# Kernel optimization log

Measured on AMD Instinct MI355X. Metric: run time of the kernel, lower is better.

Reference implementation:

```python
import jax, jax.numpy as jnp
import numpy as np

N_NODES = 10000
N_EDGES = 640000
HIDDEN = 128
N_LAYERS = 3
DECAY_RATE = 1.0


def setup_inputs() -> dict:
    key = jax.random.key(0)
    ks = jax.random.split(key, 16)
    D, L = HIDDEN, N_LAYERS
    s = 1.0 / np.sqrt(D)
    inp = {
        "x": jax.random.normal(ks[0], (N_NODES, D), dtype=jnp.float32),
        "edge_index": jax.random.randint(ks[1], (2, N_EDGES), 0, N_NODES, dtype=jnp.int32),
        "confidences": jax.random.uniform(ks[2], (N_NODES,), dtype=jnp.float32),
        # per-layer message MLP params, stacked over layers: [L, D, D] / [L, D]
        "msg_W1": jax.random.normal(ks[3], (L, D, D), dtype=jnp.float32) * s,
        "msg_b1": jnp.zeros((L, D), dtype=jnp.float32),
        "msg_W2": jax.random.normal(ks[4], (L, D, D), dtype=jnp.float32) * s,
        "msg_b2": jnp.zeros((L, D), dtype=jnp.float32),
        # per-layer self MLP params
        "self_W1": jax.random.normal(ks[5], (L, D, D), dtype=jnp.float32) * s,
        "self_b1": jnp.zeros((L, D), dtype=jnp.float32),
        "self_W2": jax.random.normal(ks[6], (L, D, D), dtype=jnp.float32) * s,
        "self_b2": jnp.zeros((L, D), dtype=jnp.float32),
        # layer-importance score net: Linear(D,D) -> ReLU -> Linear(D,1)
        "score_W1": jax.random.normal(ks[7], (D, D), dtype=jnp.float32) * s,
        "score_b1": jnp.zeros((D,), dtype=jnp.float32),
        "score_W2": jax.random.normal(ks[8], (D, 1), dtype=jnp.float32) * s,
        "score_b2": jnp.zeros((1,), dtype=jnp.float32),
    }
    return inp


def _mlp2(h, W1, b1, W2, b2):
    return jax.nn.relu(h @ W1 + b1) @ W2 + b2


def reference(x, edge_index, confidences,
              msg_W1, msg_b1, msg_W2, msg_b2,
              self_W1, self_b1, self_W2, self_b2,
              score_W1, score_b1, score_W2, score_b2):
    src, dst = edge_index[0], edge_index[1]
    # confidence-weighted edge weights: exp(-decay * |c_src - c_dst|)
    edge_weights = jnp.exp(-DECAY_RATE * jnp.abs(confidences[src] - confidences[dst]))  # [E]

    h = x
    layer_outputs = []
    for i in range(N_LAYERS):
        messages = _mlp2(h[src], msg_W1[i], msg_b1[i], msg_W2[i], msg_b2[i])  # [E, D]
        messages = messages * edge_weights[:, None]
        aggr = jax.ops.segment_sum(messages, dst, num_segments=N_NODES)  # [N, D]
        self_loop = _mlp2(h, self_W1[i], self_b1[i], self_W2[i], self_b2[i])
        h = jax.nn.relu(aggr + self_loop)  # dropout is identity in eval mode
        layer_outputs.append(h)

    stacked = jnp.stack(layer_outputs, axis=0)  # [L, N, D]
    scores = _mlp2(stacked, score_W1, score_b1, score_W2, score_b2)[..., 0]  # [L, N]
    layer_weights = jax.nn.softmax(scores, axis=0)  # softmax over layers
    output = jnp.sum(layer_weights[:, :, None] * stacked, axis=0)  # [N, D]
    return output, stacked, layer_weights
```

## Files before the change

kernel.cpp:

```cpp
#include <hip/hip_runtime.h>

#define NN 10000
#define NE 640000
#define D 128
#define NF (NN * D)
#define WS 136
#define CAP 128
#define GMB 157
#define GE ((NE + 255) / 256)
#define NAGG (NN / 4)
#define NDZ ((NN + 255) / 256)

typedef __bf16 bf16x8 __attribute__((ext_vector_type(8)));
typedef float f32x4 __attribute__((ext_vector_type(4)));


__global__ __launch_bounds__(256) void prep_kernel(
    const float* __restrict__ mW1, const float* __restrict__ mW2,
    const float* __restrict__ sW1, const float* __restrict__ sW2,
    const float* __restrict__ scW1, __bf16* __restrict__ wt, int* __restrict__ deg) {
    int b = blockIdx.x, t = threadIdx.x;
    if (b < 13) {
        int m = b;
        const float* W = (m < 3)   ? mW1 + (size_t)m * D * D
                       : (m < 6)   ? mW2 + (size_t)(m - 3) * D * D
                       : (m < 9)   ? sW1 + (size_t)(m - 6) * D * D
                       : (m < 12)  ? sW2 + (size_t)(m - 9) * D * D
                                   : scW1;
        __bf16* o = wt + (size_t)m * D * WS;
        for (int i = t; i < D * D; i += 256) {
            int k = i >> 7, n = i & 127;
            o[n * WS + k] = (__bf16)W[i];
        }
    } else {
        int i = (b - 13) * 256 + t;
        if (i < NN) deg[i] = 0;
    }
}


__device__ __forceinline__ void mlp_nostage_body(
    const __bf16* __restrict__ Abf, const float* __restrict__ Af32,
    const __bf16* __restrict__ Wt1, const float* __restrict__ b1,
    const __bf16* __restrict__ Wt2, const float* __restrict__ b2,
    __bf16* __restrict__ Mbf, float* __restrict__ Cself, int write_bf,
    __bf16 (*Tl)[16 * WS], int bx, int t) {
    int wid = t >> 6, lane = t & 63;
    int m16 = lane & 15, q = lane >> 4;
    int row0 = bx * 64 + wid * 16;
    int arow = min(row0 + m16, NN - 1);

    bf16x8 af[4];
    if (Af32) {
#pragma unroll
        for (int kk = 0; kk < 4; kk++) {
            const float4* pa = (const float4*)&Af32[(size_t)arow * D + kk * 32 + q * 8];
            float4 v0 = pa[0], v1 = pa[1];
            bf16x8 f;
            f[0] = (__bf16)v0.x; f[1] = (__bf16)v0.y; f[2] = (__bf16)v0.z; f[3] = (__bf16)v0.w;
            f[4] = (__bf16)v1.x; f[5] = (__bf16)v1.y; f[6] = (__bf16)v1.z; f[7] = (__bf16)v1.w;
            af[kk] = f;
        }
    } else {
#pragma unroll
        for (int kk = 0; kk < 4; kk++)
            af[kk] = *(const bf16x8*)&Abf[(size_t)arow * D + kk * 32 + q * 8];
    }
    float b1v[8], b2v[8];
#pragma unroll
    for (int ct = 0; ct < 8; ct++) { b1v[ct] = b1[ct * 16 + m16]; b2v[ct] = b2[ct * 16 + m16]; }

    f32x4 acc[8];
#pragma unroll
    for (int ct = 0; ct < 8; ct++) acc[ct] = (f32x4){0.f, 0.f, 0.f, 0.f};
#pragma unroll
    for (int kk = 0; kk < 4; kk++) {
#pragma unroll
        for (int ct = 0; ct < 8; ct++) {
            bf16x8 bb = *(const bf16x8*)&Wt1[(ct * 16 + m16) * WS + kk * 32 + q * 8];
            acc[ct] = __builtin_amdgcn_mfma_f32_16x16x32_bf16(af[kk], bb, acc[ct], 0, 0, 0);
        }
    }
#pragma unroll
    for (int ct = 0; ct < 8; ct++) {
#pragma unroll
        for (int r = 0; r < 4; r++) {
            float v = fmaxf(acc[ct][r] + b1v[ct], 0.f);
            Tl[wid][(q * 4 + r) * WS + ct * 16 + m16] = (__bf16)v;
        }
    }
#pragma unroll
    for (int ct = 0; ct < 8; ct++) acc[ct] = (f32x4){0.f, 0.f, 0.f, 0.f};
#pragma unroll
    for (int kk = 0; kk < 4; kk++) {
        bf16x8 a = *(const bf16x8*)&Tl[wid][m16 * WS + kk * 32 + q * 8];
#pragma unroll
        for (int ct = 0; ct < 8; ct++) {
            bf16x8 bb = *(const bf16x8*)&Wt2[(ct * 16 + m16) * WS + kk * 32 + q * 8];
            acc[ct] = __builtin_amdgcn_mfma_f32_16x16x32_bf16(a, bb, acc[ct], 0, 0, 0);
        }
    }
    if (write_bf) {
#pragma unroll
        for (int ct = 0; ct < 8; ct++) {
#pragma unroll
            for (int r = 0; r < 4; r++) {
                int row = row0 + q * 4 + r;
                if (row < NN) Mbf[(size_t)row * D + ct * 16 + m16] = (__bf16)(acc[ct][r] + b2v[ct]);
            }
        }
    } else {
#pragma unroll
        for (int ct = 0; ct < 8; ct++) {
#pragma unroll
            for (int r = 0; r < 4; r++) {
                int row = row0 + q * 4 + r;
                if (row < NN) Cself[(size_t)row * D + ct * 16 + m16] = acc[ct][r] + b2v[ct];
            }
        }
    }
}


__global__ __launch_bounds__(256) void scatter_mlp0_kernel(
    const int* __restrict__ ei, const float* __restrict__ conf,
    int* __restrict__ deg, float2* __restrict__ meta,
    const float* __restrict__ x,
    const __bf16* __restrict__ Wt1m, const float* __restrict__ b1m,
    const __bf16* __restrict__ Wt2m, const float* __restrict__ b2m, __bf16* __restrict__ Mbf,
    const __bf16* __restrict__ Wt1s, const float* __restrict__ b1s,
    const __bf16* __restrict__ Wt2s, const float* __restrict__ b2s, float* __restrict__ Cself) {
    __shared__ __align__(16) __bf16 Tl[4][16 * WS];
    int b = blockIdx.x, t = threadIdx.x;
    if (b < GMB) {
        mlp_nostage_body(nullptr, x, Wt1m, b1m, Wt2m, b2m, Mbf, nullptr, 1, Tl, b, t);
        return;
    }
    if (b < 2 * GMB) {
        mlp_nostage_body(nullptr, x, Wt1s, b1s, Wt2s, b2s, nullptr, Cself, 0, Tl, b - GMB, t);
        return;
    }
    int e = (b - 2 * GMB) * 256 + t;
    if (e < NE) {
        int s = ei[e];
        int d = ei[NE + e];
        float w = expf(-fabsf(conf[s] - conf[d]));
        int r = atomicAdd(&deg[d], 1);
        if (r < CAP) meta[(size_t)d * CAP + r] = make_float2(__int_as_float(s), w);
    }
}


__global__ __launch_bounds__(256) void aggregate_kernel(
    const uint4* __restrict__ Mbf4, const float4* __restrict__ Mself4,
    const int* __restrict__ deg, const float2* __restrict__ meta,
    float4* __restrict__ out4, bf16x8* __restrict__ stbf8) {
    int wid = (blockIdx.x * 256 + threadIdx.x) >> 6;
    int lane = threadIdx.x & 63;
    int q = lane >> 4, l4 = lane & 15, l5 = lane & 31;
    int dg = min(deg[wid], CAP);
    size_t beg = (size_t)wid * CAP;
    float a[8] = {0.f, 0.f, 0.f, 0.f, 0.f, 0.f, 0.f, 0.f};
    float2 mcur = meta[beg + l5];
    for (int rel = 0; rel < dg; rel += 32) {
        float2 mnext = meta[beg + rel + 32 + l5];
        int srcid[8];
        float wgt[8];
#pragma unroll
        for (int u = 0; u < 8; u++) {
            int sl = 4 * u + q;
            int sid = __float_as_int(__shfl(mcur.x, sl));
            float w = __shfl(mcur.y, sl);
            bool valid = (rel + sl) < dg;
            srcid[u] = valid ? sid : 0;
            wgt[u] = valid ? w : 0.f;
        }
        uint4 g[8];
#pragma unroll
        for (int u = 0; u < 8; u++) g[u] = Mbf4[(size_t)srcid[u] * 16 + l4];
#pragma unroll
        for (int u = 0; u < 8; u++) {
            float w = wgt[u];
            a[0] = fmaf(w, __uint_as_float(g[u].x << 16), a[0]);
            a[1] = fmaf(w, __uint_as_float(g[u].x & 0xFFFF0000u), a[1]);
            a[2] = fmaf(w, __uint_as_float(g[u].y << 16), a[2]);
            a[3] = fmaf(w, __uint_as_float(g[u].y & 0xFFFF0000u), a[3]);
            a[4] = fmaf(w, __uint_as_float(g[u].z << 16), a[4]);
            a[5] = fmaf(w, __uint_as_float(g[u].z & 0xFFFF0000u), a[5]);
            a[6] = fmaf(w, __uint_as_float(g[u].w << 16), a[6]);
            a[7] = fmaf(w, __uint_as_float(g[u].w & 0xFFFF0000u), a[7]);
        }
        mcur = mnext;
    }
#pragma unroll
    for (int i = 0; i < 8; i++) {
        a[i] += __shfl_xor(a[i], 16);
        a[i] += __shfl_xor(a[i], 32);
    }
    if (q == 0) {
        float4 sv0 = Mself4[(size_t)wid * 32 + 2 * l4];
        float4 sv1 = Mself4[(size_t)wid * 32 + 2 * l4 + 1];
        float4 r0, r1;
        r0.x = fmaxf(a[0] + sv0.x, 0.f);
        r0.y = fmaxf(a[1] + sv0.y, 0.f);
        r0.z = fmaxf(a[2] + sv0.z, 0.f);
        r0.w = fmaxf(a[3] + sv0.w, 0.f);
        r1.x = fmaxf(a[4] + sv1.x, 0.f);
        r1.y = fmaxf(a[5] + sv1.y, 0.f);
        r1.z = fmaxf(a[6] + sv1.z, 0.f);
        r1.w = fmaxf(a[7] + sv1.w, 0.f);
        out4[(size_t)wid * 32 + 2 * l4] = r0;
        out4[(size_t)wid * 32 + 2 * l4 + 1] = r1;
        bf16x8 hb;
        hb[0] = (__bf16)r0.x; hb[1] = (__bf16)r0.y;
        hb[2] = (__bf16)r0.z; hb[3] = (__bf16)r0.w;
        hb[4] = (__bf16)r1.x; hb[5] = (__bf16)r1.y;
        hb[6] = (__bf16)r1.z; hb[7] = (__bf16)r1.w;
        stbf8[(size_t)wid * 16 + l4] = hb;
    }
}


__global__ __launch_bounds__(256) void mlp_pair_mfma(
    const __bf16* __restrict__ Abf,
    const __bf16* __restrict__ Wt1a, const float* __restrict__ b1a,
    const __bf16* __restrict__ Wt2a, const float* __restrict__ b2a, __bf16* __restrict__ Mbf,
    const __bf16* __restrict__ Wt1b, const float* __restrict__ b1b,
    const __bf16* __restrict__ Wt2b, const float* __restrict__ b2b, float* __restrict__ Cself) {
    __shared__ __align__(16) __bf16 Tl[4][16 * WS];
    int pb = blockIdx.y;
    mlp_nostage_body(Abf, nullptr,
                     pb ? Wt1b : Wt1a, pb ? b1b : b1a,
                     pb ? Wt2b : Wt2a, pb ? b2b : b2a,
                     Mbf, Cself, pb == 0, Tl, blockIdx.x, threadIdx.x);
}


__global__ __launch_bounds__(256) void score_finalize_mfma(
    const __bf16* __restrict__ stbf, const float* __restrict__ st,
    const __bf16* __restrict__ Wt1, const float* __restrict__ b1,
    const float* __restrict__ w2, const float* __restrict__ b2,
    float* __restrict__ out, float* __restrict__ lw_out) {
    __shared__ float sc_l[3][64];
    __shared__ float lw_l[3][64];
    int t = threadIdx.x;
    int wid = t >> 6, lane = t & 63;
    int m16 = lane & 15, q = lane >> 4;
    int row0 = blockIdx.x * 64;

    int arow = min(row0 + wid * 16 + m16, NN - 1);
    float bb = b2[0];

    for (int l = 0; l < 3; l++) {
        const __bf16* A = stbf + (size_t)l * NF;
        f32x4 acc[8];
#pragma unroll
        for (int ct = 0; ct < 8; ct++) acc[ct] = (f32x4){0.f, 0.f, 0.f, 0.f};
#pragma unroll
        for (int kk = 0; kk < 4; kk++) {
            bf16x8 a = *(const bf16x8*)&A[(size_t)arow * D + kk * 32 + q * 8];
#pragma unroll
            for (int ct = 0; ct < 8; ct++) {
                bf16x8 b = *(const bf16x8*)&Wt1[(ct * 16 + m16) * WS + kk * 32 + q * 8];
                acc[ct] = __builtin_amdgcn_mfma_f32_16x16x32_bf16(a, b, acc[ct], 0, 0, 0);
            }
        }
        float p[4] = {0.f, 0.f, 0.f, 0.f};
#pragma unroll
        for (int ct = 0; ct < 8; ct++) {
            float bv = b1[ct * 16 + m16];
            float wv = w2[ct * 16 + m16];
#pragma unroll
            for (int r = 0; r < 4; r++) p[r] += fmaxf(acc[ct][r] + bv, 0.f) * wv;
        }
#pragma unroll
        for (int r = 0; r < 4; r++) {
#pragma unroll
            for (int off = 1; off < 16; off <<= 1) p[r] += __shfl_xor(p[r], off);
            if (m16 == 0) sc_l[l][wid * 16 + q * 4 + r] = p[r] + bb;
        }
    }
    __syncthreads();

    if (t < 64) {
        int row = row0 + t;
        float s0 = sc_l[0][t], s1 = sc_l[1][t], s2 = sc_l[2][t];
        float m = fmaxf(s0, fmaxf(s1, s2));
        float e0 = expf(s0 - m), e1 = expf(s1 - m), e2 = expf(s2 - m);
        float inv = 1.f / (e0 + e1 + e2);
        lw_l[0][t] = e0 * inv;
        lw_l[1][t] = e1 * inv;
        lw_l[2][t] = e2 * inv;
        if (row < NN) {
            lw_out[row] = e0 * inv;
            lw_out[NN + row] = e1 * inv;
            lw_out[2 * NN + row] = e2 * inv;
        }
    }
    __syncthreads();

    for (int i = t; i < 64 * 32; i += 256) {
        int r = i >> 5, c4 = i & 31;
        int row = row0 + r;
        if (row >= NN) break;
        float4 v0 = ((const float4*)(st + (size_t)row * D))[c4];
        float4 v1 = ((const float4*)(st + (size_t)NF + (size_t)row * D))[c4];
        float4 v2 = ((const float4*)(st + 2 * (size_t)NF + (size_t)row * D))[c4];
        float w0 = lw_l[0][r], w1 = lw_l[1][r], w2v = lw_l[2][r];
        float4 o;
        o.x = w0 * v0.x + w1 * v1.x + w2v * v2.x;
        o.y = w0 * v0.y + w1 * v1.y + w2v * v2.y;
        o.z = w0 * v0.z + w1 * v1.z + w2v * v2.z;
        o.w = w0 * v0.w + w1 * v1.w + w2v * v2.w;
        ((float4*)(out + (size_t)row * D))[c4] = o;
    }
}

extern "C" void kernel_launch(void* const* d_in, const int* in_sizes, int n_in,
                              void* d_out, int out_size, void* d_ws, size_t ws_size,
                              hipStream_t stream) {
    const float* x = (const float*)d_in[0];
    const int* ei = (const int*)d_in[1];
    const float* conf = (const float*)d_in[2];
    const float* msg_W1 = (const float*)d_in[3];
    const float* msg_b1 = (const float*)d_in[4];
    const float* msg_W2 = (const float*)d_in[5];
    const float* msg_b2 = (const float*)d_in[6];
    const float* self_W1 = (const float*)d_in[7];
    const float* self_b1 = (const float*)d_in[8];
    const float* self_W2 = (const float*)d_in[9];
    const float* self_b2 = (const float*)d_in[10];
    const float* score_W1 = (const float*)d_in[11];
    const float* score_b1 = (const float*)d_in[12];
    const float* score_W2 = (const float*)d_in[13];
    const float* score_b2 = (const float*)d_in[14];

    float* out = (float*)d_out;
    float* out_stacked = out + NF;
    float* out_lw = out + 4 * (size_t)NF;

    float* w = (float*)d_ws;
    float* Mself = w;
    float2* meta = (float2*)(w + (size_t)NF);
    __bf16* stbf = (__bf16*)(meta + (size_t)NN * CAP + 64);
    __bf16* Mbf = stbf + 3 * (size_t)NF;
    __bf16* wt = Mbf + (size_t)NF;
    int* deg = (int*)(wt + 13 * (size_t)D * WS);

    const size_t MAT = (size_t)D * WS;

    prep_kernel<<<13 + NDZ, 256, 0, stream>>>(
        msg_W1, msg_W2, self_W1, self_W2, score_W1, wt, deg);
    scatter_mlp0_kernel<<<2 * GMB + GE, 256, 0, stream>>>(
        ei, conf, deg, meta, x,
        wt + 0 * MAT, msg_b1, wt + 3 * MAT, msg_b2, Mbf,
        wt + 6 * MAT, self_b1, wt + 9 * MAT, self_b2, Mself);
    aggregate_kernel<<<NAGG, 256, 0, stream>>>(
        (const uint4*)Mbf, (const float4*)Mself, deg, meta,
        (float4*)(out_stacked + 0 * (size_t)NF), (bf16x8*)(stbf + 0 * (size_t)NF));
    for (int l = 1; l < 3; l++) {
        const __bf16* a_in = stbf + (size_t)(l - 1) * NF;
        mlp_pair_mfma<<<dim3(GMB, 2), 256, 0, stream>>>(
            a_in,
            wt + (size_t)l * MAT, msg_b1 + (size_t)l * D,
            wt + (size_t)(3 + l) * MAT, msg_b2 + (size_t)l * D, Mbf,
            wt + (size_t)(6 + l) * MAT, self_b1 + (size_t)l * D,
            wt + (size_t)(9 + l) * MAT, self_b2 + (size_t)l * D, Mself);
        aggregate_kernel<<<NAGG, 256, 0, stream>>>(
            (const uint4*)Mbf, (const float4*)Mself, deg, meta,
            (float4*)(out_stacked + (size_t)l * NF),
            (bf16x8*)(stbf + (size_t)l * NF));
    }
    score_finalize_mfma<<<GMB, 256, 0, stream>>>(
        stbf, out_stacked, wt + 12 * MAT, score_b1, score_W2, score_b2, out, out_lw);
}
```

Baseline: 238.6 us.

## Split aggregation in halves and overlap second half with next-layer MLP

Each layer's aggregation is split into two node halves. The second half runs in the same launch as the next layer's MLP (or the score pass) for the nodes already finished by the first half, and the remaining MLP or score blocks run in a follow-up kernel. Message and self-loop buffers are double-buffered so the next layer's outputs do not overwrite inputs the concurrent aggregation still reads. This is meant to fill idle CUs and hide the tail of the latency-bound gather kernel, at the cost of more launches and extra workspace.

Result: slower. 257.6 us (+8.0%).

```diff
diff --git a/kernel.cpp b/kernel.cpp
--- a/kernel.cpp
+++ b/kernel.cpp
@@ -7,8 +7,9 @@
 #define WS 136
 #define CAP 128
 #define GMB 157
+#define GMA 78
 #define GE ((NE + 255) / 256)
-#define NAGG (NN / 4)
+#define NAGH 1250
 #define NDZ ((NN + 255) / 256)
 
 typedef __bf16 bf16x8 __attribute__((ext_vector_type(8)));
@@ -122,41 +123,12 @@
 }
 
 
-__global__ __launch_bounds__(256) void scatter_mlp0_kernel(
-    const int* __restrict__ ei, const float* __restrict__ conf,
-    int* __restrict__ deg, float2* __restrict__ meta,
-    const float* __restrict__ x,
-    const __bf16* __restrict__ Wt1m, const float* __restrict__ b1m,
-    const __bf16* __restrict__ Wt2m, const float* __restrict__ b2m, __bf16* __restrict__ Mbf,
-    const __bf16* __restrict__ Wt1s, const float* __restrict__ b1s,
-    const __bf16* __restrict__ Wt2s, const float* __restrict__ b2s, float* __restrict__ Cself) {
-    __shared__ __align__(16) __bf16 Tl[4][16 * WS];
-    int b = blockIdx.x, t = threadIdx.x;
-    if (b < GMB) {
-        mlp_nostage_body(nullptr, x, Wt1m, b1m, Wt2m, b2m, Mbf, nullptr, 1, Tl, b, t);
-        return;
-    }
-    if (b < 2 * GMB) {
-        mlp_nostage_body(nullptr, x, Wt1s, b1s, Wt2s, b2s, nullptr, Cself, 0, Tl, b - GMB, t);
-        return;
-    }
-    int e = (b - 2 * GMB) * 256 + t;
-    if (e < NE) {
-        int s = ei[e];
-        int d = ei[NE + e];
-        float w = expf(-fabsf(conf[s] - conf[d]));
-        int r = atomicAdd(&deg[d], 1);
-        if (r < CAP) meta[(size_t)d * CAP + r] = make_float2(__int_as_float(s), w);
-    }
-}
-
-
-__global__ __launch_bounds__(256) void aggregate_kernel(
+__device__ __forceinline__ void aggregate_body(
     const uint4* __restrict__ Mbf4, const float4* __restrict__ Mself4,
     const int* __restrict__ deg, const float2* __restrict__ meta,
-    float4* __restrict__ out4, bf16x8* __restrict__ stbf8) {
-    int wid = (blockIdx.x * 256 + threadIdx.x) >> 6;
-    int lane = threadIdx.x & 63;
+    float4* __restrict__ out4, bf16x8* __restrict__ stbf8, int node0, int b, int t) {
+    int wid = node0 + ((b * 256 + t) >> 6);
+    int lane = t & 63;
     int q = lane >> 4, l4 = lane & 15, l5 = lane & 31;
     int dg = min(deg[wid], CAP);
     size_t beg = (size_t)wid * CAP;
@@ -221,33 +193,15 @@
 }
 
 
-__global__ __launch_bounds__(256) void mlp_pair_mfma(
-    const __bf16* __restrict__ Abf,
-    const __bf16* __restrict__ Wt1a, const float* __restrict__ b1a,
-    const __bf16* __restrict__ Wt2a, const float* __restrict__ b2a, __bf16* __restrict__ Mbf,
-    const __bf16* __restrict__ Wt1b, const float* __restrict__ b1b,
-    const __bf16* __restrict__ Wt2b, const float* __restrict__ b2b, float* __restrict__ Cself) {
-    __shared__ __align__(16) __bf16 Tl[4][16 * WS];
-    int pb = blockIdx.y;
-    mlp_nostage_body(Abf, nullptr,
-                     pb ? Wt1b : Wt1a, pb ? b1b : b1a,
-                     pb ? Wt2b : Wt2a, pb ? b2b : b2a,
-                     Mbf, Cself, pb == 0, Tl, blockIdx.x, threadIdx.x);
-}
-
-
-__global__ __launch_bounds__(256) void score_finalize_mfma(
+__device__ __forceinline__ void score_body(
+    int vb, int t, float* sc_l, float* lw_l,
     const __bf16* __restrict__ stbf, const float* __restrict__ st,
     const __bf16* __restrict__ Wt1, const float* __restrict__ b1,
     const float* __restrict__ w2, const float* __restrict__ b2,
     float* __restrict__ out, float* __restrict__ lw_out) {
-    __shared__ float sc_l[3][64];
-    __shared__ float lw_l[3][64];
-    int t = threadIdx.x;
     int wid = t >> 6, lane = t & 63;
     int m16 = lane & 15, q = lane >> 4;
-    int row0 = blockIdx.x * 64;
-
+    int row0 = vb * 64;
     int arow = min(row0 + wid * 16 + m16, NN - 1);
     float bb = b2[0];
 
@@ -277,20 +231,20 @@
         for (int r = 0; r < 4; r++) {
 #pragma unroll
             for (int off = 1; off < 16; off <<= 1) p[r] += __shfl_xor(p[r], off);
-            if (m16 == 0) sc_l[l][wid * 16 + q * 4 + r] = p[r] + bb;
+            if (m16 == 0) sc_l[l * 64 + wid * 16 + q * 4 + r] = p[r] + bb;
         }
     }
     __syncthreads();
 
     if (t < 64) {
         int row = row0 + t;
-        float s0 = sc_l[0][t], s1 = sc_l[1][t], s2 = sc_l[2][t];
+        float s0 = sc_l[0 * 64 + t], s1 = sc_l[1 * 64 + t], s2 = sc_l[2 * 64 + t];
         float m = fmaxf(s0, fmaxf(s1, s2));
         float e0 = expf(s0 - m), e1 = expf(s1 - m), e2 = expf(s2 - m);
         float inv = 1.f / (e0 + e1 + e2);
-        lw_l[0][t] = e0 * inv;
-        lw_l[1][t] = e1 * inv;
-        lw_l[2][t] = e2 * inv;
+        lw_l[0 * 64 + t] = e0 * inv;
+        lw_l[1 * 64 + t] = e1 * inv;
+        lw_l[2 * 64 + t] = e2 * inv;
         if (row < NN) {
             lw_out[row] = e0 * inv;
             lw_out[NN + row] = e1 * inv;
@@ -306,7 +260,7 @@
         float4 v0 = ((const float4*)(st + (size_t)row * D))[c4];
         float4 v1 = ((const float4*)(st + (size_t)NF + (size_t)row * D))[c4];
         float4 v2 = ((const float4*)(st + 2 * (size_t)NF + (size_t)row * D))[c4];
-        float w0 = lw_l[0][r], w1 = lw_l[1][r], w2v = lw_l[2][r];
+        float w0 = lw_l[0 * 64 + r], w1 = lw_l[1 * 64 + r], w2v = lw_l[2 * 64 + r];
         float4 o;
         o.x = w0 * v0.x + w1 * v1.x + w2v * v2.x;
         o.y = w0 * v0.y + w1 * v1.y + w2v * v2.y;
@@ -314,6 +268,115 @@
         o.w = w0 * v0.w + w1 * v1.w + w2v * v2.w;
         ((float4*)(out + (size_t)row * D))[c4] = o;
     }
+}
+
+
+__global__ __launch_bounds__(256) void scatter_mlp0_kernel(
+    const int* __restrict__ ei, const float* __restrict__ conf,
+    int* __restrict__ deg, float2* __restrict__ meta,
+    const float* __restrict__ x,
+    const __bf16* __restrict__ wt, const float* __restrict__ b1m, const float* __restrict__ b2m,
+    const float* __restrict__ b1s, const float* __restrict__ b2s,
+    __bf16* __restrict__ Mbf, float* __restrict__ Cself) {
+    __shared__ __align__(16) __bf16 Tl[4][16 * WS];
+    const size_t MAT = (size_t)D * WS;
+    int b = blockIdx.x, t = threadIdx.x;
+    if (b < GMB) {
+        mlp_nostage_body(nullptr, x, wt + 0 * MAT, b1m, wt + 3 * MAT, b2m,
+                         Mbf, nullptr, 1, Tl, b, t);
+        return;
+    }
+    if (b < 2 * GMB) {
+        mlp_nostage_body(nullptr, x, wt + 6 * MAT, b1s, wt + 9 * MAT, b2s,
+                         nullptr, Cself, 0, Tl, b - GMB, t);
+        return;
+    }
+    int e = (b - 2 * GMB) * 256 + t;
+    if (e < NE) {
+        int s = ei[e];
+        int d = ei[NE + e];
+        float w = expf(-fabsf(conf[s] - conf[d]));
+        int r = atomicAdd(&deg[d], 1);
+        if (r < CAP) meta[(size_t)d * CAP + r] = make_float2(__int_as_float(s), w);
+    }
+}
+
+
+__global__ __launch_bounds__(256) void agg_half_kernel(
+    const uint4* __restrict__ Mbf4, const float4* __restrict__ Mself4,
+    const int* __restrict__ deg, const float2* __restrict__ meta,
+    float4* __restrict__ out4, bf16x8* __restrict__ stbf8, int node0) {
+    aggregate_body(Mbf4, Mself4, deg, meta, out4, stbf8, node0, blockIdx.x, threadIdx.x);
+}
+
+
+__global__ __launch_bounds__(256) void aggB_mlpA_kernel(
+    const uint4* __restrict__ Mbf4, const float4* __restrict__ Mself4,
+    const int* __restrict__ deg, const float2* __restrict__ meta,
+    float4* __restrict__ out4, bf16x8* __restrict__ stbf8,
+    const __bf16* __restrict__ Anext,
+    const __bf16* __restrict__ Wt1m, const float* __restrict__ b1m,
+    const __bf16* __restrict__ Wt2m, const float* __restrict__ b2m, __bf16* __restrict__ MbfN,
+    const __bf16* __restrict__ Wt1s, const float* __restrict__ b1s,
+    const __bf16* __restrict__ Wt2s, const float* __restrict__ b2s, float* __restrict__ MselfN) {
+    __shared__ __align__(16) __bf16 Tl[4][16 * WS];
+    int b = blockIdx.x, t = threadIdx.x;
+    if (b < GMA) {
+        mlp_nostage_body(Anext, nullptr, Wt1m, b1m, Wt2m, b2m, MbfN, nullptr, 1, Tl, b, t);
+        return;
+    }
+    if (b < 2 * GMA) {
+        mlp_nostage_body(Anext, nullptr, Wt1s, b1s, Wt2s, b2s, nullptr, MselfN, 0, Tl, b - GMA, t);
+        return;
+    }
+    aggregate_body(Mbf4, Mself4, deg, meta, out4, stbf8, 5000, b - 2 * GMA, t);
+}
+
+
+__global__ __launch_bounds__(256) void mlpB_kernel(
+    const __bf16* __restrict__ Anext,
+    const __bf16* __restrict__ Wt1m, const float* __restrict__ b1m,
+    const __bf16* __restrict__ Wt2m, const float* __restrict__ b2m, __bf16* __restrict__ MbfN,
+    const __bf16* __restrict__ Wt1s, const float* __restrict__ b1s,
+    const __bf16* __restrict__ Wt2s, const float* __restrict__ b2s, float* __restrict__ MselfN) {
+    __shared__ __align__(16) __bf16 Tl[4][16 * WS];
+    int b = blockIdx.x, t = threadIdx.x;
+    const int NT = GMB - GMA;
+    if (b < NT)
+        mlp_nostage_body(Anext, nullptr, Wt1m, b1m, Wt2m, b2m, MbfN, nullptr, 1, Tl, GMA + b, t);
+    else
+        mlp_nostage_body(Anext, nullptr, Wt1s, b1s, Wt2s, b2s, nullptr, MselfN, 0, Tl,
+                         GMA + (b - NT), t);
+}
+
+
+__global__ __launch_bounds__(256) void aggB_scoreA_kernel(
+    const uint4* __restrict__ Mbf4, const float4* __restrict__ Mself4,
+    const int* __restrict__ deg, const float2* __restrict__ meta,
+    float4* __restrict__ out4, bf16x8* __restrict__ stbf8,
+    const __bf16* __restrict__ stbf, const float* __restrict__ st,
+    const __bf16* __restrict__ Wt1, const float* __restrict__ b1,
+    const float* __restrict__ w2, const float* __restrict__ b2,
+    float* __restrict__ out, float* __restrict__ lw_out) {
+    __shared__ float sc_l[3 * 64];
+    __shared__ float lw_l[3 * 64];
+    int b = blockIdx.x, t = threadIdx.x;
+    if (b < GMA) {
+        score_body(b, t, sc_l, lw_l, stbf, st, Wt1, b1, w2, b2, out, lw_out);
+        return;
+    }
+    aggregate_body(Mbf4, Mself4, deg, meta, out4, stbf8, 5000, b - GMA, t);
+}
+
+
+__global__ __launch_bounds__(256) void scoreB_kernel(
+    const __bf16* __restrict__ stbf, const float* __restrict__ st,
+    const __bf16* __restrict__ Wt1, const float* __restrict__ b1,
+    const float* __restrict__ w2, const float* __restrict__ b2,
+    float* __restrict__ out, float* __restrict__ lw_out) {
+    __shared__ float sc_l[3 * 64];
+    __shared__ float lw_l[3 * 64];
+    score_body(GMA + blockIdx.x, threadIdx.x, sc_l, lw_l, stbf, st, Wt1, b1, w2, b2, out, lw_out);
 }
 
 extern "C" void kernel_launch(void* const* d_in, const int* in_sizes, int n_in,
@@ -340,37 +403,53 @@
     float* out_lw = out + 4 * (size_t)NF;
 
     float* w = (float*)d_ws;
-    float* Mself = w;
-    float2* meta = (float2*)(w + (size_t)NF);
+    float* Mself0 = w;
+    float* Mself1 = Mself0 + (size_t)NF;
+    float2* meta = (float2*)(Mself1 + (size_t)NF);
     __bf16* stbf = (__bf16*)(meta + (size_t)NN * CAP + 64);
-    __bf16* Mbf = stbf + 3 * (size_t)NF;
-    __bf16* wt = Mbf + (size_t)NF;
+    __bf16* Mbf0 = stbf + 3 * (size_t)NF;
+    __bf16* Mbf1 = Mbf0 + (size_t)NF;
+    __bf16* wt = Mbf1 + (size_t)NF;
     int* deg = (int*)(wt + 13 * (size_t)D * WS);
 
     const size_t MAT = (size_t)D * WS;
+
+    __bf16* MbfL[3] = {Mbf0, Mbf1, Mbf0};
+    float* MselfL[3] = {Mself0, Mself1, Mself0};
 
     prep_kernel<<<13 + NDZ, 256, 0, stream>>>(
         msg_W1, msg_W2, self_W1, self_W2, score_W1, wt, deg);
     scatter_mlp0_kernel<<<2 * GMB + GE, 256, 0, stream>>>(
-        ei, conf, deg, meta, x,
-        wt + 0 * MAT, msg_b1, wt + 3 * MAT, msg_b2, Mbf,
-        wt + 6 * MAT, self_b1, wt + 9 * MAT, self_b2, Mself);
-    aggregate_kernel<<<NAGG, 256, 0, stream>>>(
-        (const uint4*)Mbf, (const float4*)Mself, deg, meta,
-        (float4*)(out_stacked + 0 * (size_t)NF), (bf16x8*)(stbf + 0 * (size_t)NF));
-    for (int l = 1; l < 3; l++) {
-        const __bf16* a_in = stbf + (size_t)(l - 1) * NF;
-        mlp_pair_mfma<<<dim3(GMB, 2), 256, 0, stream>>>(
-            a_in,
-            wt + (size_t)l * MAT, msg_b1 + (size_t)l * D,
-            wt + (size_t)(3 + l) * MAT, msg_b2 + (size_t)l * D, Mbf,
-            wt + (size_t)(6 + l) * MAT, self_b1 + (size_t)l * D,
-            wt + (size_t)(9 + l) * MAT, self_b2 + (size_t)l * D, Mself);
-        aggregate_kernel<<<NAGG, 256, 0, stream>>>(
-            (const uint4*)Mbf, (const float4*)Mself, deg, meta,
-            (float4*)(out_stacked + (size_t)l * NF),
-            (bf16x8*)(stbf + (size_t)l * NF));
-    }
-    score_finalize_mfma<<<GMB, 256, 0, stream>>>(
-        stbf, out_stacked, wt + 12 * MAT, score_b1, score_W2, score_b2, out, out_lw);
-}
+        ei, conf, deg, meta, x, wt, msg_b1, msg_b2, self_b1, self_b2, Mbf0, Mself0);
+
+    for (int l = 0; l < 3; l++) {
+        float4* o4 = (float4*)(out_stacked + (size_t)l * NF);
+        bf16x8* s8 = (bf16x8*)(stbf + (size_t)l * NF);
+        const uint4* mb = (const uint4*)MbfL[l];
+        const float4* ms = (const float4*)MselfL[l];
+        agg_half_kernel<<<NAGH, 256, 0, stream>>>(mb, ms, deg, meta, o4, s8, 0);
+        if (l < 2) {
+            aggB_mlpA_kernel<<<2 * GMA + NAGH, 256, 0, stream>>>(
+                mb, ms, deg, meta, o4, s8,
+                stbf + (size_t)l * NF,
+                wt + (size_t)(l + 1) * MAT, msg_b1 + (size_t)(l + 1) * D,
+                wt + (size_t)(4 + l) * MAT, msg_b2 + (size_t)(l + 1) * D, MbfL[l + 1],
+                wt + (size_t)(7 + l) * MAT, self_b1 + (size_t)(l + 1) * D,
+                wt + (size_t)(10 + l) * MAT, self_b2 + (size_t)(l + 1) * D, MselfL[l + 1]);
+            mlpB_kernel<<<2 * (GMB - GMA), 256, 0, stream>>>(
+                stbf + (size_t)l * NF,
+                wt + (size_t)(l + 1) * MAT, msg_b1 + (size_t)(l + 1) * D,
+                wt + (size_t)(4 + l) * MAT, msg_b2 + (size_t)(l + 1) * D, MbfL[l + 1],
+                wt + (size_t)(7 + l) * MAT, self_b1 + (size_t)(l + 1) * D,
+                wt + (size_t)(10 + l) * MAT, self_b2 + (size_t)(l + 1) * D, MselfL[l + 1]);
+        } else {
+            aggB_scoreA_kernel<<<GMA + NAGH, 256, 0, stream>>>(
+                mb, ms, deg, meta, o4, s8,
+                stbf, out_stacked, wt + 12 * MAT, score_b1, score_W2, score_b2,
+                out, out_lw);
+            scoreB_kernel<<<GMB - GMA, 256, 0, stream>>>(
+                stbf, out_stacked, wt + 12 * MAT, score_b1, score_W2, score_b2,
+                out, out_lw);
+        }
+    }
+}
```

## Pack edge metadata to 32-bit and fuse last aggregation with score/finalize

Applied to the files above, without the earlier changes.

Edge metadata shrinks from a float2 to a 32-bit word holding a 16-bit source id and an fp16 weight, which halves metadata traffic in every aggregation pass. The scatter blocks now come first in the combined scatter+MLP0 launch. The final aggregation is fused with the score MLP, the layer softmax and the weighted sum, so layer-2 activations stay in shared memory and one launch plus one round trip through global memory is removed. The trade-offs are fp16 precision on the edge weights, a 16-bit cap on node ids, and the score MFMA now running on 4 rows per block, which leaves most MFMA rows idle.

Result: slower. 316.0 us (+32.4%).

```diff
diff --git a/kernel.cpp b/kernel.cpp
--- a/kernel.cpp
+++ b/kernel.cpp
@@ -1,4 +1,5 @@
 #include <hip/hip_runtime.h>
+#include <hip/hip_fp16.h>
 
 #define NN 10000
 #define NE 640000
@@ -124,56 +125,60 @@
 
 __global__ __launch_bounds__(256) void scatter_mlp0_kernel(
     const int* __restrict__ ei, const float* __restrict__ conf,
-    int* __restrict__ deg, float2* __restrict__ meta,
+    int* __restrict__ deg, unsigned* __restrict__ meta,
     const float* __restrict__ x,
-    const __bf16* __restrict__ Wt1m, const float* __restrict__ b1m,
-    const __bf16* __restrict__ Wt2m, const float* __restrict__ b2m, __bf16* __restrict__ Mbf,
-    const __bf16* __restrict__ Wt1s, const float* __restrict__ b1s,
-    const __bf16* __restrict__ Wt2s, const float* __restrict__ b2s, float* __restrict__ Cself) {
+    const __bf16* __restrict__ wt, const float* __restrict__ b1m, const float* __restrict__ b2m,
+    const float* __restrict__ b1s, const float* __restrict__ b2s,
+    __bf16* __restrict__ Mbf, float* __restrict__ Cself) {
     __shared__ __align__(16) __bf16 Tl[4][16 * WS];
+    const size_t MAT = (size_t)D * WS;
     int b = blockIdx.x, t = threadIdx.x;
-    if (b < GMB) {
-        mlp_nostage_body(nullptr, x, Wt1m, b1m, Wt2m, b2m, Mbf, nullptr, 1, Tl, b, t);
+    if (b < GE) {
+        int e = b * 256 + t;
+        if (e < NE) {
+            int s = ei[e];
+            int d = ei[NE + e];
+            float w = expf(-fabsf(conf[s] - conf[d]));
+            __half h = __float2half(w);
+            unsigned short us = *reinterpret_cast<unsigned short*>(&h);
+            unsigned v = ((unsigned)s << 16) | us;
+            int r = atomicAdd(&deg[d], 1);
+            if (r < CAP) meta[(size_t)d * CAP + r] = v;
+        }
         return;
     }
-    if (b < 2 * GMB) {
-        mlp_nostage_body(nullptr, x, Wt1s, b1s, Wt2s, b2s, nullptr, Cself, 0, Tl, b - GMB, t);
-        return;
-    }
-    int e = (b - 2 * GMB) * 256 + t;
-    if (e < NE) {
-        int s = ei[e];
-        int d = ei[NE + e];
-        float w = expf(-fabsf(conf[s] - conf[d]));
-        int r = atomicAdd(&deg[d], 1);
-        if (r < CAP) meta[(size_t)d * CAP + r] = make_float2(__int_as_float(s), w);
-    }
-}
-
-
-__global__ __launch_bounds__(256) void aggregate_kernel(
-    const uint4* __restrict__ Mbf4, const float4* __restrict__ Mself4,
-    const int* __restrict__ deg, const float2* __restrict__ meta,
-    float4* __restrict__ out4, bf16x8* __restrict__ stbf8) {
-    int wid = (blockIdx.x * 256 + threadIdx.x) >> 6;
-    int lane = threadIdx.x & 63;
+    int mb = b - GE;
+    if (mb < GMB)
+        mlp_nostage_body(nullptr, x, wt + 0 * MAT, b1m, wt + 3 * MAT, b2m,
+                         Mbf, nullptr, 1, Tl, mb, t);
+    else
+        mlp_nostage_body(nullptr, x, wt + 6 * MAT, b1s, wt + 9 * MAT, b2s,
+                         nullptr, Cself, 0, Tl, mb - GMB, t);
+}
+
+
+__device__ __forceinline__ void agg_gather(
+    const uint4* __restrict__ Mbf4, const int* __restrict__ deg,
+    const unsigned* __restrict__ meta, int wid, int lane, float a[8]) {
     int q = lane >> 4, l4 = lane & 15, l5 = lane & 31;
     int dg = min(deg[wid], CAP);
     size_t beg = (size_t)wid * CAP;
-    float a[8] = {0.f, 0.f, 0.f, 0.f, 0.f, 0.f, 0.f, 0.f};
-    float2 mcur = meta[beg + l5];
+#pragma unroll
+    for (int i = 0; i < 8; i++) a[i] = 0.f;
+    unsigned mcur = meta[beg + l5];
     for (int rel = 0; rel < dg; rel += 32) {
-        float2 mnext = meta[beg + rel + 32 + l5];
+        unsigned mnext = meta[beg + rel + 32 + l5];
         int srcid[8];
         float wgt[8];
 #pragma unroll
         for (int u = 0; u < 8; u++) {
             int sl = 4 * u + q;
-            int sid = __float_as_int(__shfl(mcur.x, sl));
-            float w = __shfl(mcur.y, sl);
+            unsigned v = __shfl((int)mcur, sl);
             bool valid = (rel + sl) < dg;
-            srcid[u] = valid ? sid : 0;
-            wgt[u] = valid ? w : 0.f;
+            srcid[u] = valid ? (int)(v >> 16) : 0;
+            unsigned short us = (unsigned short)(v & 0xFFFFu);
+            __half h = *reinterpret_cast<__half*>(&us);
+            wgt[u] = valid ? __half2float(h) : 0.f;
         }
         uint4 g[8];
 #pragma unroll
@@ -197,6 +202,18 @@
         a[i] += __shfl_xor(a[i], 16);
         a[i] += __shfl_xor(a[i], 32);
     }
+}
+
+
+__global__ __launch_bounds__(256) void aggregate_kernel(
+    const uint4* __restrict__ Mbf4, const float4* __restrict__ Mself4,
+    const int* __restrict__ deg, const unsigned* __restrict__ meta,
+    float4* __restrict__ out4, bf16x8* __restrict__ stbf8) {
+    int wid = (blockIdx.x * 256 + threadIdx.x) >> 6;
+    int lane = threadIdx.x & 63;
+    int q = lane >> 4, l4 = lane & 15;
+    float a[8];
+    agg_gather(Mbf4, deg, meta, wid, lane, a);
     if (q == 0) {
         float4 sv0 = Mself4[(size_t)wid * 32 + 2 * l4];
         float4 sv1 = Mself4[(size_t)wid * 32 + 2 * l4 + 1];
@@ -236,33 +253,68 @@
 }
 
 
-__global__ __launch_bounds__(256) void score_finalize_mfma(
+__global__ __launch_bounds__(256) void agg2_score_kernel(
+    const uint4* __restrict__ Mbf4, const float4* __restrict__ Mself4,
+    const int* __restrict__ deg, const unsigned* __restrict__ meta,
+    float4* __restrict__ out4,
     const __bf16* __restrict__ stbf, const float* __restrict__ st,
     const __bf16* __restrict__ Wt1, const float* __restrict__ b1,
     const float* __restrict__ w2, const float* __restrict__ b2,
     float* __restrict__ out, float* __restrict__ lw_out) {
-    __shared__ float sc_l[3][64];
-    __shared__ float lw_l[3][64];
-    int t = threadIdx.x;
-    int wid = t >> 6, lane = t & 63;
-    int m16 = lane & 15, q = lane >> 4;
-    int row0 = blockIdx.x * 64;
-
-    int arow = min(row0 + wid * 16 + m16, NN - 1);
+    __shared__ __align__(16) __bf16 sh_h[4][D];
+    __shared__ __align__(16) float sh_f[4][D];
+    __shared__ float sc_s[3][4];
+    __shared__ float lw_s[3][4];
+    int b = blockIdx.x, t = threadIdx.x;
+    int widx = t >> 6;
+    int wid = b * 4 + widx;
+    int lane = t & 63;
+    int q = lane >> 4, m16 = lane & 15;
+
+    float a[8];
+    agg_gather(Mbf4, deg, meta, wid, lane, a);
+    if (q == 0) {
+        float4 sv0 = Mself4[(size_t)wid * 32 + 2 * m16];
+        float4 sv1 = Mself4[(size_t)wid * 32 + 2 * m16 + 1];
+        float4 r0, r1;
+        r0.x = fmaxf(a[0] + sv0.x, 0.f);
+        r0.y = fmaxf(a[1] + sv0.y, 0.f);
+        r0.z = fmaxf(a[2] + sv0.z, 0.f);
+        r0.w = fmaxf(a[3] + sv0.w, 0.f);
+        r1.x = fmaxf(a[4] + sv1.x, 0.f);
+        r1.y = fmaxf(a[5] + sv1.y, 0.f);
+        r1.z = fmaxf(a[6] + sv1.z, 0.f);
+        r1.w = fmaxf(a[7] + sv1.w, 0.f);
+        out4[(size_t)wid * 32 + 2 * m16] = r0;
+        out4[(size_t)wid * 32 + 2 * m16 + 1] = r1;
+        bf16x8 hb;
+        hb[0] = (__bf16)r0.x; hb[1] = (__bf16)r0.y;
+        hb[2] = (__bf16)r0.z; hb[3] = (__bf16)r0.w;
+        hb[4] = (__bf16)r1.x; hb[5] = (__bf16)r1.y;
+        hb[6] = (__bf16)r1.z; hb[7] = (__bf16)r1.w;
+        *(bf16x8*)&sh_h[widx][m16 * 8] = hb;
+        *(float4*)&sh_f[widx][m16 * 8] = r0;
+        *(float4*)&sh_f[widx][m16 * 8 + 4] = r1;
+    }
+    __syncthreads();
+
+    int rl = m16 & 3;
     float bb = b2[0];
-
     for (int l = 0; l < 3; l++) {
-        const __bf16* A = stbf + (size_t)l * NF;
         f32x4 acc[8];
 #pragma unroll
         for (int ct = 0; ct < 8; ct++) acc[ct] = (f32x4){0.f, 0.f, 0.f, 0.f};
 #pragma unroll
         for (int kk = 0; kk < 4; kk++) {
-            bf16x8 a = *(const bf16x8*)&A[(size_t)arow * D + kk * 32 + q * 8];
+            bf16x8 af;
+            if (l == 2)
+                af = *(const bf16x8*)&sh_h[rl][kk * 32 + q * 8];
+            else
+                af = *(const bf16x8*)&stbf[(size_t)l * NF + (size_t)(b * 4 + rl) * D + kk * 32 + q * 8];
 #pragma unroll
             for (int ct = 0; ct < 8; ct++) {
-                bf16x8 b = *(const bf16x8*)&Wt1[(ct * 16 + m16) * WS + kk * 32 + q * 8];
-                acc[ct] = __builtin_amdgcn_mfma_f32_16x16x32_bf16(a, b, acc[ct], 0, 0, 0);
+                bf16x8 bf = *(const bf16x8*)&Wt1[(ct * 16 + m16) * WS + kk * 32 + q * 8];
+                acc[ct] = __builtin_amdgcn_mfma_f32_16x16x32_bf16(af, bf, acc[ct], 0, 0, 0);
             }
         }
         float p[4] = {0.f, 0.f, 0.f, 0.f};
@@ -277,36 +329,33 @@
         for (int r = 0; r < 4; r++) {
 #pragma unroll
             for (int off = 1; off < 16; off <<= 1) p[r] += __shfl_xor(p[r], off);
-            if (m16 == 0) sc_l[l][wid * 16 + q * 4 + r] = p[r] + bb;
+            if (m16 == 0 && q == 0) sc_s[l][r] = p[r] + bb;
         }
     }
     __syncthreads();
 
-    if (t < 64) {
-        int row = row0 + t;
-        float s0 = sc_l[0][t], s1 = sc_l[1][t], s2 = sc_l[2][t];
+    if (t < 4) {
+        int row = b * 4 + t;
+        float s0 = sc_s[0][t], s1 = sc_s[1][t], s2 = sc_s[2][t];
         float m = fmaxf(s0, fmaxf(s1, s2));
         float e0 = expf(s0 - m), e1 = expf(s1 - m), e2 = expf(s2 - m);
         float inv = 1.f / (e0 + e1 + e2);
-        lw_l[0][t] = e0 * inv;
-        lw_l[1][t] = e1 * inv;
-        lw_l[2][t] = e2 * inv;
-        if (row < NN) {
-            lw_out[row] = e0 * inv;
-            lw_out[NN + row] = e1 * inv;
-            lw_out[2 * NN + row] = e2 * inv;
-        }
+        lw_s[0][t] = e0 * inv;
+        lw_s[1][t] = e1 * inv;
+        lw_s[2][t] = e2 * inv;
+        lw_out[row] = e0 * inv;
+        lw_out[NN + row] = e1 * inv;
+        lw_out[2 * NN + row] = e2 * inv;
     }
     __syncthreads();
 
-    for (int i = t; i < 64 * 32; i += 256) {
-        int r = i >> 5, c4 = i & 31;
-        int row = row0 + r;
-        if (row >= NN) break;
+    if (t < 128) {
+        int r = t >> 5, c4 = t & 31;
+        int row = b * 4 + r;
         float4 v0 = ((const float4*)(st + (size_t)row * D))[c4];
         float4 v1 = ((const float4*)(st + (size_t)NF + (size_t)row * D))[c4];
-        float4 v2 = ((const float4*)(st + 2 * (size_t)NF + (size_t)row * D))[c4];
-        float w0 = lw_l[0][r], w1 = lw_l[1][r], w2v = lw_l[2][r];
+        float4 v2 = *(const float4*)&sh_f[r][c4 * 4];
+        float w0 = lw_s[0][r], w1 = lw_s[1][r], w2v = lw_s[2][r];
         float4 o;
         o.x = w0 * v0.x + w1 * v1.x + w2v * v2.x;
         o.y = w0 * v0.y + w1 * v1.y + w2v * v2.y;
@@ -341,7 +390,7 @@
 
     float* w = (float*)d_ws;
     float* Mself = w;
-    float2* meta = (float2*)(w + (size_t)NF);
+    unsigned* meta = (unsigned*)(Mself + (size_t)NF);
     __bf16* stbf = (__bf16*)(meta + (size_t)NN * CAP + 64);
     __bf16* Mbf = stbf + 3 * (size_t)NF;
     __bf16* wt = Mbf + (size_t)NF;
@@ -351,26 +400,25 @@
 
     prep_kernel<<<13 + NDZ, 256, 0, stream>>>(
         msg_W1, msg_W2, self_W1, self_W2, score_W1, wt, deg);
-    scatter_mlp0_kernel<<<2 * GMB + GE, 256, 0, stream>>>(
-        ei, conf, deg, meta, x,
-        wt + 0 * MAT, msg_b1, wt + 3 * MAT, msg_b2, Mbf,
-        wt + 6 * MAT, self_b1, wt + 9 * MAT, self_b2, Mself);
+    scatter_mlp0_kernel<<<GE + 2 * GMB, 256, 0, stream>>>(
+        ei, conf, deg, meta, x, wt, msg_b1, msg_b2, self_b1, self_b2, Mbf, Mself);
     aggregate_kernel<<<NAGG, 256, 0, stream>>>(
         (const uint4*)Mbf, (const float4*)Mself, deg, meta,
         (float4*)(out_stacked + 0 * (size_t)NF), (bf16x8*)(stbf + 0 * (size_t)NF));
-    for (int l = 1; l < 3; l++) {
-        const __bf16* a_in = stbf + (size_t)(l - 1) * NF;
-        mlp_pair_mfma<<<dim3(GMB, 2), 256, 0, stream>>>(
-            a_in,
-            wt + (size_t)l * MAT, msg_b1 + (size_t)l * D,
-            wt + (size_t)(3 + l) * MAT, msg_b2 + (size_t)l * D, Mbf,
-            wt + (size_t)(6 + l) * MAT, self_b1 + (size_t)l * D,
-            wt + (size_t)(9 + l) * MAT, self_b2 + (size_t)l * D, Mself);
-        aggregate_kernel<<<NAGG, 256, 0, stream>>>(
-            (const uint4*)Mbf, (const float4*)Mself, deg, meta,
-            (float4*)(out_stacked + (size_t)l * NF),
-            (bf16x8*)(stbf + (size_t)l * NF));
-    }
-    score_finalize_mfma<<<GMB, 256, 0, stream>>>(
-        stbf, out_stacked, wt + 12 * MAT, score_b1, score_W2, score_b2, out, out_lw);
-}
+    mlp_pair_mfma<<<dim3(GMB, 2), 256, 0, stream>>>(
+        stbf + 0 * (size_t)NF,
+        wt + 1 * MAT, msg_b1 + D, wt + 4 * MAT, msg_b2 + D, Mbf,
+        wt + 7 * MAT, self_b1 + D, wt + 10 * MAT, self_b2 + D, Mself);
+    aggregate_kernel<<<NAGG, 256, 0, stream>>>(
+        (const uint4*)Mbf, (const float4*)Mself, deg, meta,
+        (float4*)(out_stacked + 1 * (size_t)NF), (bf16x8*)(stbf + 1 * (size_t)NF));
+    mlp_pair_mfma<<<dim3(GMB, 2), 256, 0, stream>>>(
+        stbf + 1 * (size_t)NF,
+        wt + 2 * MAT, msg_b1 + 2 * D, wt + 5 * MAT, msg_b2 + 2 * D, Mbf,
+        wt + 8 * MAT, self_b1 + 2 * D, wt + 11 * MAT, self_b2 + 2 * D, Mself);
+    agg2_score_kernel<<<NAGG, 256, 0, stream>>>(
+        (const uint4*)Mbf, (const float4*)Mself, deg, meta,
+        (float4*)(out_stacked + 2 * (size_t)NF),
+        stbf, out_stacked, wt + 12 * MAT, score_b1, score_W2, score_b2,
+        out, out_lw);
+}
```
